# Kernel optimization log

Hardware: AMD Instinct MI355X
Metric: run time of the kernel (lower is better)

## Reference

```python
import jax, jax.numpy as jnp
import numpy as np

BLOCK = 64
EPS = 1e-6
N_HEADS = 16


def _rope(t, cos, sin):
    # t: (B,S,H,hd); cos/sin: (S, hd//2) -> broadcast (1,S,1,hd//2)
    B, S, H, hd = t.shape
    tr = t.reshape(B, S, H, hd // 2, 2)
    t0, t1 = tr[..., 0], tr[..., 1]
    c = cos[None, :, None, :]
    s = sin[None, :, None, :]
    o0 = t0 * c - t1 * s
    o1 = t0 * s + t1 * c
    return jnp.stack([o0, o1], axis=-1).reshape(B, S, H, hd)


def setup_inputs() -> dict:
    key = jax.random.key(0)
    ks = jax.random.split(key, 6)
    B, S, D = 1, 2048, 2048
    hd = D // N_HEADS
    x = jax.random.normal(ks[0], (B, S, D), dtype=jnp.float32)
    # rotary table: theta_i = 10000^(-2i/hd)
    inv_freq = 1.0 / (10000.0 ** (jnp.arange(0, hd, 2, dtype=jnp.float32) / hd))
    t = jnp.arange(S, dtype=jnp.float32)
    freqs = jnp.outer(t, inv_freq)  # (S, hd//2)
    freqs_cos = jnp.cos(freqs)
    freqs_sin = jnp.sin(freqs)
    std = 0.02
    Wq = jax.random.normal(ks[1], (D, D), dtype=jnp.float32) * std
    Wk = jax.random.normal(ks[2], (D, D), dtype=jnp.float32) * std
    Wv = jax.random.normal(ks[3], (D, D), dtype=jnp.float32) * std
    Wo = jax.random.normal(ks[4], (D, D), dtype=jnp.float32) * std
    mask = jnp.ones((1, 1), dtype=bool)  # non-None mask => no masking in original code
    return {"x": x, "freqs_cos": freqs_cos, "freqs_sin": freqs_sin,
            "Wq": Wq, "Wk": Wk, "Wv": Wv, "Wo": Wo, "mask": mask}


def reference(x, freqs_cos, freqs_sin, Wq, Wk, Wv, Wo, mask):
    B, S, D = x.shape
    H = N_HEADS
    hd = D // H
    scale = hd ** -0.5
    nb = S // BLOCK

    q = (x @ Wq.T).reshape(B, S, H, hd)
    k = (x @ Wk.T).reshape(B, S, H, hd)
    v = (x @ Wv.T).reshape(B, S, H, hd)
    q = _rope(q, freqs_cos, freqs_sin)
    k = _rope(k, freqs_cos, freqs_sin)

    # block views: (B, nb, BLOCK, H, hd)
    qb = q.reshape(B, nb, BLOCK, H, hd)
    kb = k.reshape(B, nb, BLOCK, H, hd)
    vb = v.reshape(B, nb, BLOCK, H, hd)

    # per-(i,j) block scores: (B, nb_i, nb_j, H, BLOCK_q, BLOCK_k)
    s = jnp.einsum('binhd,bjmhd->bijhnm', qb, kb) * scale
    # NOTE: original module (mask is not None path) applies NO causal mask and
    # uses the per-block local max (no running-max rescale) -- reproduced exactly.
    m = jnp.max(s, axis=-1, keepdims=True)
    p = jnp.exp(s - m)
    # denominator: sum of per-block row sums over all j blocks -> (B, nb, H, BLOCK)
    L = p.sum(axis=-1).sum(axis=2)
    # numerator: sum over j blocks of p @ v -> (B, nb, BLOCK, H, hd)
    O = jnp.einsum('bijhnm,bjmhd->binhd', p, vb).reshape(B, S, H, hd)
    Lr = L.transpose(0, 1, 3, 2).reshape(B, S, H, 1)  # (B,S,H,1)
    O = O / (Lr + EPS)
    return O.reshape(B, S, D) @ Wo.T
```

## Files before the change

### kernel.cpp

```cpp
#include <hip/hip_runtime.h>
#include <hip/hip_bf16.h>
#include <math.h>

#define SEQ 2048
#define DM  2048
#define NH  16
#define HD  128
#define SCALE 0.08838834764831845f

typedef __bf16 bf16_t;
typedef __bf16 bf16x8 __attribute__((ext_vector_type(8)));
typedef __bf16 bf16x4 __attribute__((ext_vector_type(4)));
typedef float  f32x4  __attribute__((ext_vector_type(4)));
typedef int    i32x4  __attribute__((ext_vector_type(4)));

typedef const __attribute__((address_space(1))) void* gas_ptr;
typedef __attribute__((address_space(3))) void* las_ptr;

__device__ __forceinline__ void gload_lds16(const void* g, void* l) {
    __builtin_amdgcn_global_load_lds((gas_ptr)g, (las_ptr)l, 16, 0, 0);
}

__device__ __forceinline__ f32x4 mfma_bf16(bf16x8 a, bf16x8 b, f32x4 c) {
    return __builtin_amdgcn_mfma_f32_16x16x32_bf16(a, b, c, 0, 0, 0);
}

__device__ __forceinline__ unsigned cvtpk_bf16(float lo, float hi) {
    unsigned d;
    asm("v_cvt_pk_bf16_f32 %0, %1, %2" : "=v"(d) : "v"(lo), "v"(hi));
    return d;
}

__device__ __forceinline__ bf16x8 read_frag64(const bf16_t* lds, int row, int k) {
    int chunk = (k >> 3) ^ (row & 7);
    return *(const bf16x8*)(lds + row * 64 + chunk * 8);
}
__device__ __forceinline__ bf16x8 read_frag128(const bf16_t* lds, int row, int k) {
    int chunk = k >> 3;
    chunk = (chunk & 8) | ((chunk ^ row) & 7);
    return *(const bf16x8*)(lds + row * 128 + chunk * 8);
}
__device__ __forceinline__ bf16x8 read_slab(const bf16_t* sl, int row, int g) {
    int j = g ^ ((row >> 1) & 3);
    return *(const bf16x8*)(sl + row * 32 + j * 8);
}

__global__ __launch_bounds__(256) void cvt5(
    const float* __restrict__ s0, const float* __restrict__ s1,
    const float* __restrict__ s2, const float* __restrict__ s3,
    const float* __restrict__ s4,
    bf16_t* __restrict__ d0, bf16_t* __restrict__ d1, bf16_t* __restrict__ d2,
    bf16_t* __restrict__ d3, bf16_t* __restrict__ d4)
{
    int which = blockIdx.y;
    const float* s; bf16_t* d;
    switch (which) {
        case 0: s = s0; d = d0; break;
        case 1: s = s1; d = d1; break;
        case 2: s = s2; d = d2; break;
        case 3: s = s3; d = d3; break;
        default: s = s4; d = d4; break;
    }
    size_t idx = ((size_t)blockIdx.x * 256 + threadIdx.x) * 4;
    float4 v = *(const float4*)(s + idx);
    bf16x4 o = { (bf16_t)v.x, (bf16_t)v.y, (bf16_t)v.z, (bf16_t)v.w };
    *(bf16x4*)(d + idx) = o;
}

#define BARX() asm volatile("s_barrier" ::: "memory")
#define VMW8 asm volatile("s_waitcnt vmcnt(8)" ::: "memory")
#define VMW4 asm volatile("s_waitcnt vmcnt(4)" ::: "memory")
#define VMW0 asm volatile("s_waitcnt vmcnt(0)" ::: "memory")
#define NOGATE

__global__ __launch_bounds__(512, 2) void qkv_pipe(
    const bf16_t* __restrict__ A,
    const bf16_t* __restrict__ B0, const bf16_t* __restrict__ B1,
    const bf16_t* __restrict__ B2,
    bf16_t* __restrict__ Oq, bf16_t* __restrict__ Ok, bf16_t* __restrict__ Ov,
    const float* __restrict__ fcos, const float* __restrict__ fsin)
{
    __shared__ bf16_t lds[65536];

    const int tid = threadIdx.x;
    const int lane = tid & 63;
    const int w = tid >> 6;
    const int wm = w >> 2;
    const int wn = w & 3;
    const int g4 = lane >> 4, r15 = lane & 15;

    const int bm = blockIdx.y;
    const int bny = blockIdx.x;
    const int sel = bny >> 3;
    const int bnl = bny & 7;
    const bf16_t* Bp = (sel == 0) ? B0 : (sel == 1) ? B1 : B2;

    const size_t arow0 = (size_t)bm * 256;
    const size_t brow0 = (size_t)bnl * 256;

    const int row0 = tid >> 2;
    const int kj0  = (tid & 3) ^ ((row0 >> 1) & 3);
    const bf16_t* pA = A  + (arow0 + row0) * DM + kj0 * 8;
    const bf16_t* pB = Bp + (brow0 + row0) * DM + kj0 * 8;
    char* ldsb = (char*)lds;
    const int off0 = tid * 16;
    const int off1 = 8192 + tid * 16;

    #define STAGE_HT(S) do { if ((S) < 128) {                                   \
        const int T_ = (S) >> 2, a_ = (S) & 3;                                  \
        const int ko_ = T_ * 64 + ((a_ >> 1) << 5);                             \
        char* dst_ = ldsb + (((T_ & 1) << 16) | ((a_ & 1) << 15) | ((a_ >> 1) << 14)); \
        const bf16_t* s0_ = (a_ & 1) ? pB : pA;                                 \
        gload_lds16(s0_ + ko_, dst_ + off0);                                    \
        gload_lds16(s0_ + 128 * DM + ko_, dst_ + off1);                         \
    } } while (0)

    const bf16_t* b0A0 = lds;
    const bf16_t* b0A1 = lds + 8192;
    const bf16_t* b0B0 = lds + 16384;
    const bf16_t* b0B1 = lds + 24576;
    const bf16_t* b1A0 = lds + 32768;
    const bf16_t* b1A1 = lds + 40960;
    const bf16_t* b1B0 = lds + 49152;
    const bf16_t* b1B1 = lds + 57344;

    f32x4 acc[8][4] = {};

    #define PHASE(ASL, BSL, MH, SIDX, GATE, READB)                              \
    {                                                                           \
        _Pragma("unroll")                                                       \
        for (int m = 0; m < 4; ++m)                                             \
            af[m] = read_slab((ASL), wm * 128 + (MH) * 64 + m * 16 + r15, g4);  \
        if (READB) {                                                            \
            _Pragma("unroll")                                                   \
            for (int n = 0; n < 4; ++n)                                         \
                bfr[n] = read_slab((BSL), wn * 64 + n * 16 + r15, g4);          \
        }                                                                       \
        STAGE_HT(SIDX);                                                         \
        GATE;                                                                   \
        BARX();                                                                 \
        __builtin_amdgcn_s_setprio(1);                                          \
        _Pragma("unroll")                                                       \
        for (int m = 0; m < 4; ++m)                                             \
            _Pragma("unroll")                                                   \
            for (int n = 0; n < 4; ++n)                                         \
                acc[(MH) * 4 + m][n] = mfma_bf16(af[m], bfr[n], acc[(MH) * 4 + m][n]); \
        __builtin_amdgcn_s_setprio(0);                                          \
        BARX();                                                                 \
    }

    STAGE_HT(0); STAGE_HT(1); STAGE_HT(2); STAGE_HT(3); STAGE_HT(4); STAGE_HT(5);
    VMW8;
    BARX();

    for (int i = 0; i < 15; ++i) {
        const int s0 = 6 + i * 8;
        bf16x8 af[4], bfr[4];
        PHASE(b0A0, b0B0, 0, s0 + 0, NOGATE, 1)
        PHASE(b0A0, b0B0, 1, s0 + 1, VMW8,   0)
        PHASE(b0A1, b0B1, 0, s0 + 2, NOGATE, 1)
        PHASE(b0A1, b0B1, 1, s0 + 3, VMW8,   0)
        PHASE(b1A0, b1B0, 0, s0 + 4, NOGATE, 1)
        PHASE(b1A0, b1B0, 1, s0 + 5, VMW8,   0)
        PHASE(b1A1, b1B1, 0, s0 + 6, NOGATE, 1)
        PHASE(b1A1, b1B1, 1, s0 + 7, VMW8,   0)
    }
    {
        const int s0 = 6 + 15 * 8;
        bf16x8 af[4], bfr[4];
        PHASE(b0A0, b0B0, 0, s0 + 0, NOGATE, 1)
        PHASE(b0A0, b0B0, 1, s0 + 1, VMW8,   0)
        PHASE(b0A1, b0B1, 0, s0 + 2, NOGATE, 1)
        PHASE(b0A1, b0B1, 1, s0 + 3, VMW4,   0)
        PHASE(b1A0, b1B0, 0, s0 + 4, NOGATE, 1)
        PHASE(b1A0, b1B0, 1, s0 + 5, VMW0,   0)
        PHASE(b1A1, b1B1, 0, s0 + 6, NOGATE, 1)
        PHASE(b1A1, b1B1, 1, s0 + 7, NOGATE, 0)
    }
    #undef PHASE
    #undef STAGE_HT

    const int r0 = bm * 256 + wm * 128;
    const int c0 = bnl * 256 + wn * 64;

    if (sel == 2) {
        #pragma unroll
        for (int m = 0; m < 8; ++m) {
            int rowb = r0 + m * 16 + g4 * 4;
            #pragma unroll
            for (int n = 0; n < 4; ++n) {
                int col = c0 + n * 16 + r15;
                bf16x4 pk = { (bf16_t)acc[m][n][0], (bf16_t)acc[m][n][1],
                              (bf16_t)acc[m][n][2], (bf16_t)acc[m][n][3] };
                *(bf16x4*)&Ov[(size_t)col * SEQ + rowb] = pk;
            }
        }
    } else {
        bf16_t* dst = (sel == 0) ? Oq : Ok;
        #pragma unroll
        for (int m = 0; m < 8; ++m) {
            int rowb = r0 + m * 16 + g4 * 4;
            #pragma unroll
            for (int n = 0; n < 4; ++n) {
                int col = c0 + n * 16 + r15;
                int f = (col & (HD - 1)) >> 1;
                float sgn = (col & 1) ? 1.0f : -1.0f;
                #pragma unroll
                for (int r = 0; r < 4; ++r) {
                    float mine = acc[m][n][r];
                    float other = __shfl_xor(mine, 1);
                    float cc = fcos[(rowb + r) * (HD / 2) + f];
                    float ss = fsin[(rowb + r) * (HD / 2) + f];
                    float o = mine * cc + sgn * other * ss;
                    dst[(size_t)(rowb + r) * DM + col] = (bf16_t)o;
                }
            }
        }
    }
}

__global__ __launch_bounds__(256) void gemm_fin(
    const bf16_t* __restrict__ A, const bf16_t* __restrict__ B0,
    float* __restrict__ Of)
{
    __shared__ bf16_t lA[128 * 64];
    __shared__ bf16_t lB[64 * 64];

    const int tid = threadIdx.x;
    const int lane = tid & 63;
    const int w = tid >> 6;
    const int wm = w >> 1, wn = w & 1;
    const int g = lane >> 4, r15 = lane & 15;

    const int bm = blockIdx.x;
    const int bn = blockIdx.y;

    f32x4 acc[4][2] = {};

    const size_t arow0 = (size_t)bm * 128;
    const size_t brow0 = (size_t)bn * 64;

    for (int kt = 0; kt < DM / 64; ++kt) {
        const int k0 = kt * 64;
        #pragma unroll
        for (int i = 0; i < 4; ++i) {
            int c = i * 256 + tid;
            int row = c >> 3;
            int ck = (c ^ row) & 7;
            const bf16_t* ga = A + (arow0 + row) * DM + k0 + ck * 8;
            gload_lds16(ga, (char*)lA + (i * 256 + w * 64) * 16);
        }
        #pragma unroll
        for (int i = 0; i < 2; ++i) {
            int c = i * 256 + tid;
            int row = c >> 3;
            int ck = (c ^ row) & 7;
            const bf16_t* gb = B0 + (brow0 + row) * DM + k0 + ck * 8;
            gload_lds16(gb, (char*)lB + (i * 256 + w * 64) * 16);
        }
        __syncthreads();
        #pragma unroll
        for (int kk = 0; kk < 2; ++kk) {
            bf16x8 af[4], bfr[2];
            #pragma unroll
            for (int m = 0; m < 4; ++m)
                af[m] = read_frag64(lA, wm * 64 + m * 16 + r15, kk * 32 + g * 8);
            #pragma unroll
            for (int n = 0; n < 2; ++n)
                bfr[n] = read_frag64(lB, wn * 32 + n * 16 + r15, kk * 32 + g * 8);
            #pragma unroll
            for (int m = 0; m < 4; ++m)
                #pragma unroll
                for (int n = 0; n < 2; ++n)
                    acc[m][n] = mfma_bf16(af[m], bfr[n], acc[m][n]);
        }
        __syncthreads();
    }

    const int r0 = bm * 128 + wm * 64;
    const int c0 = bn * 64 + wn * 32;
    #pragma unroll
    for (int m = 0; m < 4; ++m) {
        int rowb = r0 + m * 16 + g * 4;
        #pragma unroll
        for (int n = 0; n < 2; ++n) {
            int col = c0 + n * 16 + r15;
            #pragma unroll
            for (int r = 0; r < 4; ++r)
                Of[(size_t)(rowb + r) * DM + col] = acc[m][n][r];
        }
    }
}

__global__ __launch_bounds__(256, 2) void attn_k5(
    const bf16_t* __restrict__ Q, const bf16_t* __restrict__ Kb,
    const bf16_t* __restrict__ Vt, bf16_t* __restrict__ Ob)
{
    __shared__ bf16_t lk[2 * 64 * 128];
    __shared__ bf16_t lv[2 * 128 * 64];

    const int tid = threadIdx.x;
    const int lane = tid & 63;
    const int w = tid >> 6;
    const int g = lane >> 4, r15 = lane & 15;
    const int qb = blockIdx.x, h = blockIdx.y;

    const int lo = g & 1, hb = g >> 1;
    const int e_src = (lo << 5) + r15;
    const int o_src = e_src + 16;
    const int sA = hb ? o_src : e_src;
    const int sB = hb ? e_src : o_src;

    bf16x8 qf[2][4];
    #pragma unroll
    for (int u = 0; u < 2; ++u) {
        const bf16_t* qrow = Q + (size_t)(qb * 128 + w * 32 + u * 16 + r15) * DM + h * HD + g * 8;
        #pragma unroll
        for (int ks = 0; ks < 4; ++ks)
            qf[u][ks] = *(const bf16x8*)(qrow + ks * 32);
    }

    f32x4 oacc[2][8] = {};
    float Lsum[2] = {0.f, 0.f};

    #define STAGE_KV(JJ, BUF)                                                     \
    {                                                                             \
        _Pragma("unroll")                                                         \
        for (int i = 0; i < 4; ++i) {                                             \
            int c = i * 256 + tid;                                                \
            int row = c >> 4, ckl = c & 15;                                       \
            int ck = (ckl & 8) | ((ckl ^ row) & 7);                               \
            const bf16_t* gk = Kb + (size_t)((JJ) * 64 + row) * DM + h * HD + ck * 8; \
            gload_lds16(gk, (char*)lk + (BUF) * 16384 + (i * 256 + w * 64) * 16); \
        }                                                                         \
        _Pragma("unroll")                                                         \
        for (int i = 0; i < 4; ++i) {                                             \
            int c = i * 256 + tid;                                                \
            int row = c >> 3;                                                     \
            int ck = (c ^ row) & 7;                                               \
            const bf16_t* gv = Vt + (size_t)(h * HD + row) * SEQ + (JJ) * 64 + ck * 8; \
            gload_lds16(gv, (char*)lv + (BUF) * 16384 + (i * 256 + w * 64) * 16); \
        }                                                                         \
    }

    STAGE_KV(0, 0);
    asm volatile("s_waitcnt vmcnt(0)" ::: "memory");
    __builtin_amdgcn_s_barrier();

    for (int j = 0; j < SEQ / 64; ++j) {
        const int cur = j & 1;
        const bf16_t* lkc = lk + cur * 8192;
        const bf16_t* lvc = lv + cur * 8192;
        if (j < SEQ / 64 - 1) STAGE_KV(j + 1, cur ^ 1);

        f32x4 sacc[2][4] = {};
        __builtin_amdgcn_s_setprio(1);
        #pragma unroll
        for (int ks = 0; ks < 4; ++ks) {
            #pragma unroll
            for (int n = 0; n < 4; ++n) {
                bf16x8 kf = read_frag128(lkc, n * 16 + r15, ks * 32 + g * 8);
                sacc[0][n] = mfma_bf16(kf, qf[0][ks], sacc[0][n]);
                sacc[1][n] = mfma_bf16(kf, qf[1][ks], sacc[1][n]);
            }
        }
        __builtin_amdgcn_s_setprio(0);

        bf16x8 pa0[2], pa1[2];
        #pragma unroll
        for (int u = 0; u < 2; ++u) {
            float mx0 = fmaxf(fmaxf(sacc[u][0][0], sacc[u][0][1]), fmaxf(sacc[u][0][2], sacc[u][0][3]));
            float mx1 = fmaxf(fmaxf(sacc[u][1][0], sacc[u][1][1]), fmaxf(sacc[u][1][2], sacc[u][1][3]));
            float mx2 = fmaxf(fmaxf(sacc[u][2][0], sacc[u][2][1]), fmaxf(sacc[u][2][2], sacc[u][2][3]));
            float mx3 = fmaxf(fmaxf(sacc[u][3][0], sacc[u][3][1]), fmaxf(sacc[u][3][2], sacc[u][3][3]));
            float mx = fmaxf(fmaxf(mx0, mx1), fmaxf(mx2, mx3));
            mx = fmaxf(mx, __shfl_xor(mx, 16));
            mx = fmaxf(mx, __shfl_xor(mx, 32));

            float p[4][4];
            float ls = 0.f;
            #pragma unroll
            for (int n = 0; n < 4; ++n)
                #pragma unroll
                for (int r = 0; r < 4; ++r) {
                    float pv = __expf((sacc[u][n][r] - mx) * SCALE);
                    p[n][r] = pv;
                    ls += pv;
                }
            Lsum[u] += ls;

            unsigned D00 = cvtpk_bf16(p[0][0], p[0][1]), D01 = cvtpk_bf16(p[0][2], p[0][3]);
            unsigned D10 = cvtpk_bf16(p[1][0], p[1][1]), D11 = cvtpk_bf16(p[1][2], p[1][3]);
            unsigned D20 = cvtpk_bf16(p[2][0], p[2][1]), D21 = cvtpk_bf16(p[2][2], p[2][3]);
            unsigned D30 = cvtpk_bf16(p[3][0], p[3][1]), D31 = cvtpk_bf16(p[3][2], p[3][3]);

            unsigned r0 = __shfl((int)(lo ? D10 : D00), sA);
            unsigned r1 = __shfl((int)(lo ? D11 : D01), sA);
            unsigned r2 = __shfl((int)(lo ? D00 : D10), sB);
            unsigned r3 = __shfl((int)(lo ? D01 : D11), sB);
            unsigned r4 = __shfl((int)(lo ? D30 : D20), sA);
            unsigned r5 = __shfl((int)(lo ? D31 : D21), sA);
            unsigned r6 = __shfl((int)(lo ? D20 : D30), sB);
            unsigned r7 = __shfl((int)(lo ? D21 : D31), sB);
            i32x4 w0, w1;
            w0[0] = (int)(hb ? r2 : r0);  w0[1] = (int)(hb ? r3 : r1);
            w0[2] = (int)(hb ? r0 : r2);  w0[3] = (int)(hb ? r1 : r3);
            w1[0] = (int)(hb ? r6 : r4);  w1[1] = (int)(hb ? r7 : r5);
            w1[2] = (int)(hb ? r4 : r6);  w1[3] = (int)(hb ? r5 : r7);
            pa0[u] = __builtin_bit_cast(bf16x8, w0);
            pa1[u] = __builtin_bit_cast(bf16x8, w1);
        }

        __builtin_amdgcn_s_setprio(1);
        #pragma unroll
        for (int n = 0; n < 8; ++n) {
            bf16x8 bv0 = read_frag64(lvc, n * 16 + r15, g * 8);
            oacc[0][n] = mfma_bf16(pa0[0], bv0, oacc[0][n]);
            oacc[1][n] = mfma_bf16(pa0[1], bv0, oacc[1][n]);
            bf16x8 bv1 = read_frag64(lvc, n * 16 + r15, 32 + g * 8);
            oacc[0][n] = mfma_bf16(pa1[0], bv1, oacc[0][n]);
            oacc[1][n] = mfma_bf16(pa1[1], bv1, oacc[1][n]);
        }
        __builtin_amdgcn_s_setprio(0);

        asm volatile("s_waitcnt vmcnt(0)" ::: "memory");
        __builtin_amdgcn_s_barrier();
    }

    #pragma unroll
    for (int u = 0; u < 2; ++u) {
        float L = Lsum[u];
        L += __shfl_xor(L, 16);
        L += __shfl_xor(L, 32);
        float inv = 1.0f / (L + 1e-6f);
        float invr[4];
        #pragma unroll
        for (int r = 0; r < 4; ++r)
            invr[r] = __shfl(inv, g * 4 + r);

        #pragma unroll
        for (int n = 0; n < 8; ++n) {
            int col = h * HD + n * 16 + r15;
            int rowb = qb * 128 + w * 32 + u * 16 + g * 4;
            #pragma unroll
            for (int r = 0; r < 4; ++r)
                Ob[(size_t)(rowb + r) * DM + col] = (bf16_t)(oacc[u][n][r] * invr[r]);
        }
    }
}

extern "C" void kernel_launch(void* const* d_in, const int* in_sizes, int n_in,
                              void* d_out, int out_size, void* d_ws, size_t ws_size,
                              hipStream_t stream)
{
    const float* x    = (const float*)d_in[0];
    const float* fcos = (const float*)d_in[1];
    const float* fsin = (const float*)d_in[2];
    const float* Wq   = (const float*)d_in[3];
    const float* Wk   = (const float*)d_in[4];
    const float* Wv   = (const float*)d_in[5];
    const float* Wo   = (const float*)d_in[6];
    float* out = (float*)d_out;

    const size_t NE = (size_t)DM * SEQ;
    bf16_t* ws  = (bf16_t*)d_ws;
    bf16_t* xb  = ws;
    bf16_t* wqb = ws + 1 * NE;
    bf16_t* wkb = ws + 2 * NE;
    bf16_t* wvb = ws + 3 * NE;
    bf16_t* wob = ws + 4 * NE;
    bf16_t* qr  = ws + 5 * NE;
    bf16_t* kr  = ws + 6 * NE;
    bf16_t* vt  = ws + 7 * NE;
    bf16_t* ob  = ws + 8 * NE;

    hipLaunchKernelGGL(cvt5, dim3(4096, 5), dim3(256), 0, stream,
                       x, Wq, Wk, Wv, Wo, xb, wqb, wkb, wvb, wob);

    hipLaunchKernelGGL(qkv_pipe, dim3(24, 8), dim3(512), 0, stream,
                       xb, wqb, wkb, wvb, qr, kr, vt, fcos, fsin);

    hipLaunchKernelGGL(attn_k5, dim3(16, 16), dim3(256), 0, stream,
                       qr, kr, vt, ob);

    hipLaunchKernelGGL(gemm_fin, dim3(16, 32), dim3(256), 0, stream,
                       ob, wob, out);
}
```

Measured before the change: 181.0 us.

## Split attention KV range across blocks and add a partial-sum combine kernel

The attention kernel now splits the 32 KV blocks into 4 chunks along a new grid dimension. It uses 512-thread blocks that each cover 256 query rows, and writes unnormalized bf16 partial outputs and per-row partial denominators to the workspace. A new combine kernel sums the 4 partials, divides by the total denominator plus eps and writes the normalized bf16 output. The goal is more concurrent work per CU and better occupancy than one block per CU running a long serial KV loop. The cost is an extra kernel launch, extra global traffic for the partials, and some added rounding from storing the partials in bf16.

```diff
diff --git a/kernel.cpp b/kernel.cpp
--- a/kernel.cpp
+++ b/kernel.cpp
@@ -292,9 +292,10 @@
     }
 }
 
-__global__ __launch_bounds__(256, 2) void attn_k5(
+__global__ __launch_bounds__(512, 2) void attn_k6(
     const bf16_t* __restrict__ Q, const bf16_t* __restrict__ Kb,
-    const bf16_t* __restrict__ Vt, bf16_t* __restrict__ Ob)
+    const bf16_t* __restrict__ Vt, bf16_t* __restrict__ Op,
+    float* __restrict__ Lp)
 {
     __shared__ bf16_t lk[2 * 64 * 128];
     __shared__ bf16_t lv[2 * 128 * 64];
@@ -303,7 +304,10 @@
     const int lane = tid & 63;
     const int w = tid >> 6;
     const int g = lane >> 4, r15 = lane & 15;
-    const int qb = blockIdx.x, h = blockIdx.y;
+    const int qb = blockIdx.x;
+    const int h = blockIdx.y;
+    const int sp = blockIdx.z;
+    const int j0 = sp * 8;
 
     const int lo = g & 1, hb = g >> 1;
     const int e_src = (lo << 5) + r15;
@@ -314,7 +318,7 @@
     bf16x8 qf[2][4];
     #pragma unroll
     for (int u = 0; u < 2; ++u) {
-        const bf16_t* qrow = Q + (size_t)(qb * 128 + w * 32 + u * 16 + r15) * DM + h * HD + g * 8;
+        const bf16_t* qrow = Q + (size_t)(qb * 256 + w * 32 + u * 16 + r15) * DM + h * HD + g * 8;
         #pragma unroll
         for (int ks = 0; ks < 4; ++ks)
             qf[u][ks] = *(const bf16x8*)(qrow + ks * 32);
@@ -326,32 +330,32 @@
     #define STAGE_KV(JJ, BUF)                                                     \
     {                                                                             \
         _Pragma("unroll")                                                         \
-        for (int i = 0; i < 4; ++i) {                                             \
-            int c = i * 256 + tid;                                                \
+        for (int i = 0; i < 2; ++i) {                                             \
+            int c = i * 512 + tid;                                                \
             int row = c >> 4, ckl = c & 15;                                       \
             int ck = (ckl & 8) | ((ckl ^ row) & 7);                               \
             const bf16_t* gk = Kb + (size_t)((JJ) * 64 + row) * DM + h * HD + ck * 8; \
-            gload_lds16(gk, (char*)lk + (BUF) * 16384 + (i * 256 + w * 64) * 16); \
+            gload_lds16(gk, (char*)lk + (BUF) * 16384 + (i * 512 + w * 64) * 16); \
         }                                                                         \
         _Pragma("unroll")                                                         \
-        for (int i = 0; i < 4; ++i) {                                             \
-            int c = i * 256 + tid;                                                \
+        for (int i = 0; i < 2; ++i) {                                             \
+            int c = i * 512 + tid;                                                \
             int row = c >> 3;                                                     \
             int ck = (c ^ row) & 7;                                               \
             const bf16_t* gv = Vt + (size_t)(h * HD + row) * SEQ + (JJ) * 64 + ck * 8; \
-            gload_lds16(gv, (char*)lv + (BUF) * 16384 + (i * 256 + w * 64) * 16); \
+            gload_lds16(gv, (char*)lv + (BUF) * 16384 + (i * 512 + w * 64) * 16); \
         }                                                                         \
     }
 
-    STAGE_KV(0, 0);
+    STAGE_KV(j0, 0);
     asm volatile("s_waitcnt vmcnt(0)" ::: "memory");
     __builtin_amdgcn_s_barrier();
 
-    for (int j = 0; j < SEQ / 64; ++j) {
-        const int cur = j & 1;
+    for (int jj = 0; jj < 8; ++jj) {
+        const int cur = jj & 1;
         const bf16_t* lkc = lk + cur * 8192;
         const bf16_t* lvc = lv + cur * 8192;
-        if (j < SEQ / 64 - 1) STAGE_KV(j + 1, cur ^ 1);
+        if (jj < 7) STAGE_KV(j0 + jj + 1, cur ^ 1);
 
         f32x4 sacc[2][4] = {};
         __builtin_amdgcn_s_setprio(1);
@@ -432,21 +436,48 @@
         float L = Lsum[u];
         L += __shfl_xor(L, 16);
         L += __shfl_xor(L, 32);
-        float inv = 1.0f / (L + 1e-6f);
-        float invr[4];
-        #pragma unroll
-        for (int r = 0; r < 4; ++r)
-            invr[r] = __shfl(inv, g * 4 + r);
+        int qrow = qb * 256 + w * 32 + u * 16;
+        if (g == 0)
+            Lp[((size_t)sp * NH + h) * SEQ + qrow + r15] = L;
 
         #pragma unroll
         for (int n = 0; n < 8; ++n) {
             int col = h * HD + n * 16 + r15;
-            int rowb = qb * 128 + w * 32 + u * 16 + g * 4;
+            int rowb = qrow + g * 4;
             #pragma unroll
             for (int r = 0; r < 4; ++r)
-                Ob[(size_t)(rowb + r) * DM + col] = (bf16_t)(oacc[u][n][r] * invr[r]);
-        }
-    }
+                Op[(size_t)sp * SEQ * DM + (size_t)(rowb + r) * DM + col] = (bf16_t)oacc[u][n][r];
+        }
+    }
+}
+
+__global__ __launch_bounds__(256) void attn_cmb(
+    const bf16_t* __restrict__ Op, const float* __restrict__ Lp,
+    bf16_t* __restrict__ Ob)
+{
+    const int row = blockIdx.x;
+    const int c0 = threadIdx.x * 8;
+    const int h = c0 >> 7;
+
+    float L = 1e-6f;
+    #pragma unroll
+    for (int s = 0; s < 4; ++s)
+        L += Lp[((size_t)s * NH + h) * SEQ + row];
+
+    float acc[8] = {};
+    #pragma unroll
+    for (int s = 0; s < 4; ++s) {
+        bf16x8 v = *(const bf16x8*)(Op + (size_t)s * SEQ * DM + (size_t)row * DM + c0);
+        #pragma unroll
+        for (int j = 0; j < 8; ++j)
+            acc[j] += (float)v[j];
+    }
+    float inv = 1.0f / L;
+    bf16x8 o;
+    #pragma unroll
+    for (int j = 0; j < 8; ++j)
+        o[j] = (bf16_t)(acc[j] * inv);
+    *(bf16x8*)(Ob + (size_t)row * DM + c0) = o;
 }
 
 extern "C" void kernel_launch(void* const* d_in, const int* in_sizes, int n_in,
@@ -473,6 +504,8 @@
     bf16_t* kr  = ws + 6 * NE;
     bf16_t* vt  = ws + 7 * NE;
     bf16_t* ob  = ws + 8 * NE;
+    bf16_t* op  = ws;
+    float*  lp  = (float*)(ws + 9 * NE);
 
     hipLaunchKernelGGL(cvt5, dim3(4096, 5), dim3(256), 0, stream,
                        x, Wq, Wk, Wv, Wo, xb, wqb, wkb, wvb, wob);
@@ -480,8 +513,11 @@
     hipLaunchKernelGGL(qkv_pipe, dim3(24, 8), dim3(512), 0, stream,
                        xb, wqb, wkb, wvb, qr, kr, vt, fcos, fsin);
 
-    hipLaunchKernelGGL(attn_k5, dim3(16, 16), dim3(256), 0, stream,
-                       qr, kr, vt, ob);
+    hipLaunchKernelGGL(attn_k6, dim3(8, 16, 4), dim3(512), 0, stream,
+                       qr, kr, vt, op, lp);
+
+    hipLaunchKernelGGL(attn_cmb, dim3(2048), dim3(256), 0, stream,
+                       op, lp, ob);
 
     hipLaunchKernelGGL(gemm_fin, dim3(16, 32), dim3(256), 0, stream,
                        ob, wob, out);
```

New measurement: 176.3 us. 1.03x faster.
